# Optimization experiments

Measured on AMD Instinct MI355X. Metric: run time of the kernel, lower is better.

Reference implementation:

```python
import jax, jax.numpy as jnp
import numpy as np

B, N_HM, K_APP, S = 16, 32, 16, 256

def setup_inputs() -> dict:
    key = jax.random.key(0)
    k1, k2, k3 = jax.random.split(key, 3)
    # x: post-UNet appearance feature map [B, K, S, S]
    x = jax.random.normal(k1, (B, K_APP, S, S), dtype=jnp.float32)
    # raw_tps: raw heatmap logits [B, N, S, S]
    raw_tps = jax.random.normal(k2, (B, N_HM, S, S), dtype=jnp.float32)
    # fitted_cj: non-negative fitted heatmaps [B, N, S, S]
    fitted_cj = jax.random.uniform(k3, (B, N_HM, S, S), dtype=jnp.float32)
    return {"x": x, "raw_tps": raw_tps, "fitted_cj": fitted_cj}

def reference(x, raw_tps, fitted_cj):
    # torch F.softmax on a 2D [S,S] tensor with no dim defaults to dim=1 -> per-row softmax
    p = jax.nn.softmax(raw_tps, axis=-1)                      # [B, N, S, S]
    # attention pooling: app_vec[b,n,k] = sum_{h,w} x[b,k,h,w] * p[b,n,h,w]
    app_vec = jnp.einsum('bkhw,bnhw->bnk', x, p)              # [B, N, K]
    # weighted combine without materializing the [B,N,S,S,K] repeat
    num = jnp.einsum('bnhw,bnk->bhwk', fitted_cj, app_vec)    # [B, S, S, K]
    denom = 1.0 + jnp.sum(fitted_cj, axis=1)[..., None]       # [B, S, S, 1]
    app_enco = num / denom                                     # [B, S, S, K]
    # transpose(2,3) then transpose(1,2): [B,S,S,K] -> [B,K,S,S]
    return jnp.transpose(app_enco, (0, 3, 1, 2))
```

## Files before the change

### kernel.cpp

```cpp
#include <hip/hip_runtime.h>

#define S_DIM 256
#define N_HM 32
#define K_APP 16
#define LDW 264

typedef __bf16 b16x8 __attribute__((ext_vector_type(8)));
typedef float  f32x4 __attribute__((ext_vector_type(4)));

__device__ __forceinline__ unsigned short f2bf(float f) {
    unsigned u = __builtin_bit_cast(unsigned, f);
    unsigned r = u + 0x7FFFu + ((u >> 16) & 1u);
    return (unsigned short)(r >> 16);
}
__device__ __forceinline__ float bf2f(unsigned short s) {
    return __builtin_bit_cast(float, (unsigned)s << 16);
}

template <bool ATOMIC>
__global__ __launch_bounds__(256, 2) void k1_softmax_pool(
    const float* __restrict__ x,
    const float* __restrict__ raw,
    float* __restrict__ outp)
{
    __shared__ unsigned short eA[4][16][LDW];
    __shared__ unsigned short xH[2][16][LDW];
    __shared__ unsigned short xL[2][16][LDW];

    const int tid  = threadIdx.x;
    const int wv   = tid >> 6;
    const int lane = tid & 63;
    const int hsel = wv & 1;
    const int rg   = wv >> 1;
    const int u    = (blockIdx.x << 1) + hsel;
    const int b    = u >> 8;
    const int h    = u & 255;

    {
        const float* xb = x + ((size_t)(b * K_APP + rg * 8) << 16) + (h << 8) + (lane << 2);
        #pragma unroll
        for (int q = 0; q < 8; ++q) {
            float4 v = *(const float4*)(xb + ((size_t)q << 16));
            const int k = rg * 8 + q;
            unsigned short h0 = f2bf(v.x), h1 = f2bf(v.y), h2 = f2bf(v.z), h3 = f2bf(v.w);
            unsigned short l0 = f2bf(v.x - bf2f(h0)), l1 = f2bf(v.y - bf2f(h1));
            unsigned short l2 = f2bf(v.z - bf2f(h2)), l3 = f2bf(v.w - bf2f(h3));
            *(ushort4*)&xH[hsel][k][lane << 2] = make_ushort4(h0, h1, h2, h3);
            *(ushort4*)&xL[hsel][k][lane << 2] = make_ushort4(l0, l1, l2, l3);
        }
    }

    {
        const float* rb = raw + ((size_t)(b * N_HM + rg * 16) << 16) + (h << 8) + (lane << 2);
        #pragma unroll
        for (int i = 0; i < 16; ++i) {
            float4 v = *(const float4*)(rb + ((size_t)i << 16));
            *(ushort4*)&eA[wv][i][lane << 2] =
                make_ushort4(f2bf(__expf(v.x)), f2bf(__expf(v.y)),
                             f2bf(__expf(v.z)), f2bf(__expf(v.w)));
        }
    }
    __syncthreads();

    f32x4 acc  = {0.f, 0.f, 0.f, 0.f};
    f32x4 sacc = {0.f, 0.f, 0.f, 0.f};
    b16x8 ones;
    #pragma unroll
    for (int j = 0; j < 8; ++j) ones[j] = (__bf16)1.0f;

    const int frow = lane & 15;
    const int fcol = (lane >> 4) << 3;

    #pragma unroll
    for (int st = 0; st < 8; ++st) {
        b16x8 a  = *(const b16x8*)&eA[wv][frow][fcol + (st << 5)];
        b16x8 bh = *(const b16x8*)&xH[hsel][frow][fcol + (st << 5)];
        b16x8 bl = *(const b16x8*)&xL[hsel][frow][fcol + (st << 5)];
        acc  = __builtin_amdgcn_mfma_f32_16x16x32_bf16(a, bh, acc, 0, 0, 0);
        acc  = __builtin_amdgcn_mfma_f32_16x16x32_bf16(a, bl, acc, 0, 0, 0);
        sacc = __builtin_amdgcn_mfma_f32_16x16x32_bf16(a, ones, sacc, 0, 0, 0);
    }

    #pragma unroll
    for (int r = 0; r < 4; ++r) {
        const int rowl = ((lane >> 4) << 2) + r;
        const int n    = (rg << 4) + rowl;
        const float v  = acc[r] * __builtin_amdgcn_rcpf(sacc[r]);
        if (ATOMIC) {
            atomicAdd(outp + (b << 9) + (n << 4) + (lane & 15), v);
        } else {
            outp[((size_t)u << 9) + (n << 4) + (lane & 15)] = v;
        }
    }
}

__global__ __launch_bounds__(256) void k1_reduce(
    const float* __restrict__ partial, float* __restrict__ av)
{
    __shared__ float s_lds[256];
    const int tid = threadIdx.x;
    const int o   = (blockIdx.x << 5) + (tid & 31);
    const int ch  = tid >> 5;
    const int b   = o >> 9;
    const int r   = o & 511;

    const float* p = partial + ((size_t)((b << 8) + (ch << 5)) << 9) + r;
    float s = 0.0f;
    #pragma unroll 8
    for (int j = 0; j < 32; ++j) s += p[(size_t)j << 9];

    s_lds[tid] = s;
    __syncthreads();
    if (tid < 32) {
        float t = s_lds[tid];
        #pragma unroll
        for (int c = 1; c < 8; ++c) t += s_lds[tid + (c << 5)];
        av[o] = t;
    }
}

__global__ __launch_bounds__(256, 4) void k2_combine(
    const float* __restrict__ fit,
    const float* __restrict__ av,
    float* __restrict__ out)
{
    const int tid = threadIdx.x;
    const int b   = blockIdx.x >> 6;
    const int hw4 = ((blockIdx.x & 63) << 8) + tid;

    const float*  avb = av + (b << 9);
    const float4* fb  = (const float4*)fit + ((size_t)(b * N_HM) << 14) + hw4;

    float4 num[16];
    #pragma unroll
    for (int k = 0; k < 16; ++k) num[k] = make_float4(0.f, 0.f, 0.f, 0.f);
    float dx = 1.f, dy = 1.f, dz = 1.f, dw = 1.f;

#define ACC(K, AS)                                                         \
    num[K].x += f.x * (AS); num[K].y += f.y * (AS);                        \
    num[K].z += f.z * (AS); num[K].w += f.w * (AS);

    #pragma unroll 8
    for (int n = 0; n < N_HM; ++n) {
        float4 f = fb[(size_t)n << 14];
        dx += f.x; dy += f.y; dz += f.z; dw += f.w;
        const float4* ar = (const float4*)(avb + (n << 4));
        float4 a0 = ar[0], a1 = ar[1], a2 = ar[2], a3 = ar[3];
        ACC(0,  a0.x) ACC(1,  a0.y) ACC(2,  a0.z) ACC(3,  a0.w)
        ACC(4,  a1.x) ACC(5,  a1.y) ACC(6,  a1.z) ACC(7,  a1.w)
        ACC(8,  a2.x) ACC(9,  a2.y) ACC(10, a2.z) ACC(11, a2.w)
        ACC(12, a3.x) ACC(13, a3.y) ACC(14, a3.z) ACC(15, a3.w)
    }
#undef ACC

    const float ix = 1.f / dx, iy = 1.f / dy, iz = 1.f / dz, iw = 1.f / dw;
    float4* ob = (float4*)out + ((size_t)(b * K_APP) << 14) + hw4;
    #pragma unroll
    for (int k = 0; k < 16; ++k)
        ob[(size_t)k << 14] = make_float4(num[k].x * ix, num[k].y * iy,
                                          num[k].z * iz, num[k].w * iw);
}

extern "C" void kernel_launch(void* const* d_in, const int* in_sizes, int n_in,
                              void* d_out, int out_size, void* d_ws, size_t ws_size,
                              hipStream_t stream)
{
    const float* x   = (const float*)d_in[0];
    const float* raw = (const float*)d_in[1];
    const float* fit = (const float*)d_in[2];
    float* out = (float*)d_out;

    float* av      = (float*)d_ws;
    float* partial = (float*)d_ws + 8192;
    const size_t need = (size_t)(8192 + 4096 * 512) * sizeof(float);

    if (ws_size >= need) {
        k1_softmax_pool<false><<<2048, 256, 0, stream>>>(x, raw, partial);
        k1_reduce<<<256, 256, 0, stream>>>(partial, av);
    } else {
        hipMemsetAsync(av, 0, 8192 * sizeof(float), stream);
        k1_softmax_pool<true><<<2048, 256, 0, stream>>>(x, raw, av);
    }
    k2_combine<<<1024, 256, 0, stream>>>(fit, av, out);
}
```

Before: 340.5 us.

## Load MFMA fragments directly from global memory, removing LDS staging

The softmax-pool kernel no longer stages exp(raw) and the hi/lo bf16 split of x through shared memory. Each lane now loads its own MFMA fragment straight from global memory and converts it in registers, which removes the LDS buffers and the block barrier. With no LDS use, the launch-bounds occupancy hint goes from 2 to 6 blocks per CU. The cost is duplicated global loads of x across the two row-group waves and smaller, strided per-lane loads instead of fully coalesced rows.

```diff
diff --git a/kernel.cpp b/kernel.cpp
--- a/kernel.cpp
+++ b/kernel.cpp
@@ -3,30 +3,16 @@
 #define S_DIM 256
 #define N_HM 32
 #define K_APP 16
-#define LDW 264
 
 typedef __bf16 b16x8 __attribute__((ext_vector_type(8)));
 typedef float  f32x4 __attribute__((ext_vector_type(4)));
 
-__device__ __forceinline__ unsigned short f2bf(float f) {
-    unsigned u = __builtin_bit_cast(unsigned, f);
-    unsigned r = u + 0x7FFFu + ((u >> 16) & 1u);
-    return (unsigned short)(r >> 16);
-}
-__device__ __forceinline__ float bf2f(unsigned short s) {
-    return __builtin_bit_cast(float, (unsigned)s << 16);
-}
-
 template <bool ATOMIC>
-__global__ __launch_bounds__(256, 2) void k1_softmax_pool(
+__global__ __launch_bounds__(256, 6) void k1_softmax_pool(
     const float* __restrict__ x,
     const float* __restrict__ raw,
     float* __restrict__ outp)
 {
-    __shared__ unsigned short eA[4][16][LDW];
-    __shared__ unsigned short xH[2][16][LDW];
-    __shared__ unsigned short xL[2][16][LDW];
-
     const int tid  = threadIdx.x;
     const int wv   = tid >> 6;
     const int lane = tid & 63;
@@ -36,31 +22,11 @@
     const int b    = u >> 8;
     const int h    = u & 255;
 
-    {
-        const float* xb = x + ((size_t)(b * K_APP + rg * 8) << 16) + (h << 8) + (lane << 2);
-        #pragma unroll
-        for (int q = 0; q < 8; ++q) {
-            float4 v = *(const float4*)(xb + ((size_t)q << 16));
-            const int k = rg * 8 + q;
-            unsigned short h0 = f2bf(v.x), h1 = f2bf(v.y), h2 = f2bf(v.z), h3 = f2bf(v.w);
-            unsigned short l0 = f2bf(v.x - bf2f(h0)), l1 = f2bf(v.y - bf2f(h1));
-            unsigned short l2 = f2bf(v.z - bf2f(h2)), l3 = f2bf(v.w - bf2f(h3));
-            *(ushort4*)&xH[hsel][k][lane << 2] = make_ushort4(h0, h1, h2, h3);
-            *(ushort4*)&xL[hsel][k][lane << 2] = make_ushort4(l0, l1, l2, l3);
-        }
-    }
+    const int frow = lane & 15;
+    const int fcol = (lane >> 4) << 3;
 
-    {
-        const float* rb = raw + ((size_t)(b * N_HM + rg * 16) << 16) + (h << 8) + (lane << 2);
-        #pragma unroll
-        for (int i = 0; i < 16; ++i) {
-            float4 v = *(const float4*)(rb + ((size_t)i << 16));
-            *(ushort4*)&eA[wv][i][lane << 2] =
-                make_ushort4(f2bf(__expf(v.x)), f2bf(__expf(v.y)),
-                             f2bf(__expf(v.z)), f2bf(__expf(v.w)));
-        }
-    }
-    __syncthreads();
+    const float* abase = raw + ((size_t)(b * N_HM  + (rg << 4) + frow) << 16) + (h << 8) + fcol;
+    const float* bbase = x   + ((size_t)(b * K_APP + frow)             << 16) + (h << 8) + fcol;
 
     f32x4 acc  = {0.f, 0.f, 0.f, 0.f};
     f32x4 sacc = {0.f, 0.f, 0.f, 0.f};
@@ -68,16 +34,28 @@
     #pragma unroll
     for (int j = 0; j < 8; ++j) ones[j] = (__bf16)1.0f;
 
-    const int frow = lane & 15;
-    const int fcol = (lane >> 4) << 3;
-
     #pragma unroll
     for (int st = 0; st < 8; ++st) {
-        b16x8 a  = *(const b16x8*)&eA[wv][frow][fcol + (st << 5)];
-        b16x8 bh = *(const b16x8*)&xH[hsel][frow][fcol + (st << 5)];
-        b16x8 bl = *(const b16x8*)&xL[hsel][frow][fcol + (st << 5)];
-        acc  = __builtin_amdgcn_mfma_f32_16x16x32_bf16(a, bh, acc, 0, 0, 0);
-        acc  = __builtin_amdgcn_mfma_f32_16x16x32_bf16(a, bl, acc, 0, 0, 0);
+        float4 ra0 = *(const float4*)(abase + (st << 5));
+        float4 ra1 = *(const float4*)(abase + (st << 5) + 4);
+        float4 xv0 = *(const float4*)(bbase + (st << 5));
+        float4 xv1 = *(const float4*)(bbase + (st << 5) + 4);
+
+        float e0 = __expf(ra0.x), e1 = __expf(ra0.y), e2 = __expf(ra0.z), e3 = __expf(ra0.w);
+        float e4 = __expf(ra1.x), e5 = __expf(ra1.y), e6 = __expf(ra1.z), e7 = __expf(ra1.w);
+        b16x8 a = { (__bf16)e0, (__bf16)e1, (__bf16)e2, (__bf16)e3,
+                    (__bf16)e4, (__bf16)e5, (__bf16)e6, (__bf16)e7 };
+
+        __bf16 h0 = (__bf16)xv0.x, h1 = (__bf16)xv0.y, h2 = (__bf16)xv0.z, h3 = (__bf16)xv0.w;
+        __bf16 h4 = (__bf16)xv1.x, h5 = (__bf16)xv1.y, h6 = (__bf16)xv1.z, h7 = (__bf16)xv1.w;
+        b16x8 bh = { h0, h1, h2, h3, h4, h5, h6, h7 };
+        b16x8 bl = { (__bf16)(xv0.x - (float)h0), (__bf16)(xv0.y - (float)h1),
+                     (__bf16)(xv0.z - (float)h2), (__bf16)(xv0.w - (float)h3),
+                     (__bf16)(xv1.x - (float)h4), (__bf16)(xv1.y - (float)h5),
+                     (__bf16)(xv1.z - (float)h6), (__bf16)(xv1.w - (float)h7) };
+
+        acc  = __builtin_amdgcn_mfma_f32_16x16x32_bf16(a, bh,   acc,  0, 0, 0);
+        acc  = __builtin_amdgcn_mfma_f32_16x16x32_bf16(a, bl,   acc,  0, 0, 0);
         sacc = __builtin_amdgcn_mfma_f32_16x16x32_bf16(a, ones, sacc, 0, 0, 0);
     }
 
```

Result: slower. 350.1 us (+2.8%).
